# Kernel tuning notes

Measured on AMD Instinct MI355X. Metric: run time of the kernel, lower is better.

Reference implementation:

```python
import jax, jax.numpy as jnp
import numpy as np

N_NODES = 100000
N_EDGES = 600000
N_ETYPES = 3
N_LAYERS = 3  # n_layers + 1 conv layers
D = 128
EPS = 1e-5


def setup_inputs() -> dict:
    key = jax.random.key(0)
    ks = jax.random.split(key, 8)
    scale = 1.0 / np.sqrt(D)
    x = jax.random.normal(ks[0], (N_NODES, D), dtype=jnp.float32)
    src = jax.random.randint(ks[1], (N_ETYPES, N_EDGES), 0, N_NODES, dtype=jnp.int32)
    dst = jax.random.randint(ks[2], (N_ETYPES, N_EDGES), 0, N_NODES, dtype=jnp.int32)
    W_self = jax.random.normal(ks[3], (N_LAYERS, N_ETYPES, D, D), dtype=jnp.float32) * scale
    W_neigh = jax.random.normal(ks[4], (N_LAYERS, N_ETYPES, D, D), dtype=jnp.float32) * scale
    b = jax.random.normal(ks[5], (N_LAYERS, N_ETYPES, D), dtype=jnp.float32) * 0.01
    gamma = jnp.ones((N_LAYERS, D), dtype=jnp.float32)
    beta = jnp.zeros((N_LAYERS, D), dtype=jnp.float32)
    return {"x": x, "src": src, "dst": dst, "W_self": W_self, "W_neigh": W_neigh,
            "b": b, "gamma": gamma, "beta": beta}


def reference(x, src, dst, W_self, W_neigh, b, gamma, beta):
    N = x.shape[0]
    L, K = W_self.shape[0], W_self.shape[1]
    # in-degree per etype (DGL mean aggregator: zero-degree -> 0 neighbor feat)
    degs = [jnp.clip(jax.ops.segment_sum(jnp.ones((dst.shape[1],), x.dtype), dst[k],
                                         num_segments=N), 1.0, None)
            for k in range(K)]
    h = x
    for l in range(L):
        acc = jnp.zeros((N, W_self.shape[-1]), x.dtype)
        for k in range(K):
            # gather src feats, mean-aggregate onto dst: [N, D]
            neigh = jax.ops.segment_sum(h[src[k]], dst[k], num_segments=N) / degs[k][:, None]
            o = h @ W_self[l, k] + neigh @ W_neigh[l, k] + b[l, k]
            if l < L - 1:  # activation inside SAGEConv, last layer has none
                o = jax.nn.relu(o)
            acc = acc + o  # HeteroGraphConv aggregate='sum'
        # BatchNorm1d, training mode (biased batch variance)
        mu = acc.mean(axis=0)
        var = ((acc - mu) ** 2).mean(axis=0)
        h = gamma[l] * (acc - mu) / jnp.sqrt(var + EPS) + beta[l]
    return h
```

## Files before the change

### kernel.cpp

```cpp
#include <hip/hip_runtime.h>

#define NN 100000
#define NNP 100096
#define NE 600000
#define KE 3
#define NL 3
#define D  128
#define EPS 1e-5f
#define NB 391
#define NBKT 196
#define EPB 4096
#define NEB 147
#define NSL 16

typedef __attribute__((ext_vector_type(8))) short short8;
typedef __attribute__((ext_vector_type(4))) float floatx4;

__device__ __forceinline__ void atomic_add_f32(float* p, float v) { unsafeAtomicAdd(p, v); }

__device__ __forceinline__ float bf2f(unsigned int u16) {
    unsigned int v = u16 << 16;
    return __builtin_bit_cast(float, v);
}
__device__ __forceinline__ unsigned int f2bf(float f) {
    unsigned int u = __builtin_bit_cast(unsigned int, f);
    u += 0x7FFFu + ((u >> 16) & 1u);
    return u >> 16;
}
__device__ __forceinline__ unsigned int pack2(float a, float b) {
    return f2bf(a) | (f2bf(b) << 16);
}

__device__ __forceinline__ void gload16(const void* g, void* l) {
    __builtin_amdgcn_global_load_lds(
        (const __attribute__((address_space(1))) void*)g,
        (__attribute__((address_space(3))) void*)l, 16, 0, 0);
}

__global__ void convert_x_kernel(const float* __restrict__ x, ushort* __restrict__ hbf) {
    size_t i = (size_t)blockIdx.x * blockDim.x + threadIdx.x;
    if (i >= (size_t)NN * D / 4) return;
    float4 v = *(const float4*)(x + i * 4);
    uint2 o;
    o.x = pack2(v.x, v.y);
    o.y = pack2(v.z, v.w);
    *(uint2*)(hbf + i * 4) = o;
}

__global__ void wprep_kernel(const float* __restrict__ Ws, const float* __restrict__ Wn,
                             ushort* __restrict__ Bt) {
    int idx = blockIdx.x * blockDim.x + threadIdx.x;
    if (idx >= NL * KE * 128 * 256) return;
    int lk  = idx >> 15;
    int rem = idx & 32767;
    int n   = rem >> 8;
    int kk  = rem & 255;
    float v = (kk < 128) ? Ws[(size_t)lk * 16384 + kk * 128 + n]
                         : Wn[(size_t)lk * 16384 + (kk - 128) * 128 + n];
    Bt[idx] = (ushort)f2bf(v);
}

__global__ void fold_kernel(const float* __restrict__ Wsl, const float* __restrict__ bsrc,
                            const float* __restrict__ ssl, ushort* __restrict__ Btl,
                            float* __restrict__ biasW) {
    const int k = blockIdx.x;
    const int n = threadIdx.x;
    const float* W = Wsl + (size_t)k * D * D;
    ushort* B = Btl + (size_t)k * 32768;
    float acc = 0.f;
    #pragma unroll 4
    for (int kk = 0; kk < D; ++kk) {
        float w = W[kk * D + n];
        acc += ssl[D + kk] * w;
        B[n * 256 + kk] = (ushort)f2bf(ssl[kk] * w);
    }
    biasW[k * D + n] = bsrc[k * D + n] + acc;
}

__global__ void bucket_count_kernel(const int* __restrict__ dst,
                                    int* __restrict__ bucketTotal, int* __restrict__ blockBase) {
    const int blk = blockIdx.x;
    const int k = blk / NEB, cb = blk - k * NEB;
    __shared__ int hist[NBKT];
    for (int i = threadIdx.x; i < NBKT; i += 256) hist[i] = 0;
    __syncthreads();
    const int e0 = cb * EPB, e1 = min(e0 + EPB, NE);
    for (int e = e0 + threadIdx.x; e < e1; e += 256)
        atomicAdd(&hist[dst[(size_t)k * NE + e] >> 9], 1);
    __syncthreads();
    for (int i = threadIdx.x; i < NBKT; i += 256) {
        int c = hist[i];
        int base = c ? atomicAdd(&bucketTotal[k * NBKT + i], c) : 0;
        blockBase[(size_t)blk * NBKT + i] = base;
    }
}

__global__ void bucket_scan_kernel(const int* __restrict__ bucketTotal,
                                   int* __restrict__ bucketStart) {
    __shared__ int sd[1024];
    const int t = threadIdx.x;
    int v = (t < KE * NBKT) ? bucketTotal[t] : 0;
    sd[t] = v;
    __syncthreads();
    for (int off = 1; off < 1024; off <<= 1) {
        int u = (t >= off) ? sd[t - off] : 0;
        __syncthreads();
        sd[t] += u;
        __syncthreads();
    }
    if (t < KE * NBKT) bucketStart[t] = sd[t] - v;
}

__global__ void bucket_scatter_kernel(const int* __restrict__ src, const int* __restrict__ dst,
                                      const int* __restrict__ bucketStart,
                                      const int* __restrict__ blockBase,
                                      uint2* __restrict__ ebuf) {
    const int blk = blockIdx.x;
    const int k = blk / NEB, cb = blk - k * NEB;
    __shared__ int hist[NBKT], binoff[NBKT], cur[NBKT];
    __shared__ int sc[256];
    __shared__ uint2 stage[EPB];
    const int t = threadIdx.x;
    for (int i = t; i < NBKT; i += 256) hist[i] = 0;
    __syncthreads();
    const int e0 = cb * EPB, e1 = min(e0 + EPB, NE);
    for (int e = e0 + t; e < e1; e += 256)
        atomicAdd(&hist[dst[(size_t)k * NE + e] >> 9], 1);
    __syncthreads();
    int hv = (t < NBKT) ? hist[t] : 0;
    sc[t] = hv;
    __syncthreads();
    for (int off = 1; off < 256; off <<= 1) {
        int u = (t >= off) ? sc[t - off] : 0;
        __syncthreads();
        sc[t] += u;
        __syncthreads();
    }
    if (t < NBKT) { binoff[t] = sc[t] - hv; cur[t] = sc[t] - hv; }
    __syncthreads();
    for (int e = e0 + t; e < e1; e += 256) {
        int d = dst[(size_t)k * NE + e], s = src[(size_t)k * NE + e];
        int b = d >> 9;
        int p = atomicAdd(&cur[b], 1);
        stage[p] = make_uint2((unsigned)s, (unsigned)d);
    }
    __syncthreads();
    const int n = e1 - e0;
    for (int i = t; i < n; i += 256) {
        uint2 ed = stage[i];
        int b = (int)(ed.y >> 9);
        int pos = bucketStart[k * NBKT + b] + blockBase[(size_t)blk * NBKT + b] + (i - binoff[b]);
        ebuf[pos] = ed;
    }
}

__global__ void bucket_deg_kernel(const uint2* __restrict__ ebuf,
                                  const int* __restrict__ bucketStart, int* __restrict__ degi) {
    const int blk = blockIdx.x;
    const int k = blk / NBKT, b = blk - k * NBKT;
    __shared__ int cnt[512];
    for (int i = threadIdx.x; i < 512; i += 256) cnt[i] = 0;
    __syncthreads();
    const int s0 = bucketStart[blk];
    const int s1 = (blk + 1 < KE * NBKT) ? bucketStart[blk + 1] : KE * NE;
    for (int e = s0 + threadIdx.x; e < s1; e += 256)
        atomicAdd(&cnt[ebuf[e].y & 511], 1);
    __syncthreads();
    const int n0 = b << 9;
    for (int i = threadIdx.x; i < 512; i += 256) {
        int node = n0 + i;
        if (node < NN) degi[(size_t)k * NN + node] = cnt[i];
    }
}

__global__ void scan_a_kernel(const int* __restrict__ degi, int* __restrict__ bsum) {
    const int b = blockIdx.x;
    const int k = b / NB, lb = b - k * NB;
    const int t = threadIdx.x;
    const int i = lb * 256 + t;
    int deg = (i < NN) ? degi[(size_t)k * NN + i] : 0;
    __shared__ int sd[256];
    sd[t] = deg;
    __syncthreads();
    for (int off = 128; off > 0; off >>= 1) {
        if (t < off) sd[t] += sd[t + off];
        __syncthreads();
    }
    if (t == 0) bsum[b] = sd[0];
}

__global__ void scan_b_kernel(int* __restrict__ bsum) {
    const int k = blockIdx.x;
    const int t = threadIdx.x;
    int v = (t < NB) ? bsum[k * NB + t] : 0;
    __shared__ int sd[512];
    sd[t] = v;
    __syncthreads();
    for (int off = 1; off < 512; off <<= 1) {
        int u = (t >= off) ? sd[t - off] : 0;
        __syncthreads();
        sd[t] += u;
        __syncthreads();
    }
    if (t < NB) bsum[k * NB + t] = sd[t] - v;
}

__global__ void scan_c_kernel(const int* __restrict__ degi, const int* __restrict__ bsum,
                              int* __restrict__ rowptr, float* __restrict__ invdeg) {
    const int b = blockIdx.x;
    const int k = b / NB, lb = b - k * NB;
    const int t = threadIdx.x;
    const int i = lb * 256 + t;
    int deg = (i < NN) ? degi[(size_t)k * NN + i] : 0;
    __shared__ int sd[256];
    sd[t] = deg;
    __syncthreads();
    for (int off = 1; off < 256; off <<= 1) {
        int u = (t >= off) ? sd[t - off] : 0;
        __syncthreads();
        sd[t] += u;
        __syncthreads();
    }
    int val = bsum[b] + sd[t] - deg;
    if (i < NN) {
        rowptr[(size_t)k * (NN + 1) + i] = val;
        invdeg[(size_t)k * NN + i] = 1.0f / (float)max(deg, 1);
    }
    if (i == NN) rowptr[(size_t)k * (NN + 1) + NN] = NE;
}

__global__ void bucket_fill_kernel(const uint2* __restrict__ ebuf,
                                   const int* __restrict__ bucketStart,
                                   const int* __restrict__ rowptr, int* __restrict__ csr) {
    const int blk = blockIdx.x;
    const int k = blk / NBKT, b = blk - k * NBKT;
    __shared__ int cur[512];
    const int n0 = b << 9;
    for (int i = threadIdx.x; i < 512; i += 256) {
        int node = n0 + i;
        cur[i] = (node < NN) ? rowptr[(size_t)k * (NN + 1) + node] : 0;
    }
    __syncthreads();
    const int s0 = bucketStart[blk];
    const int s1 = (blk + 1 < KE * NBKT) ? bucketStart[blk + 1] : KE * NE;
    for (int e = s0 + threadIdx.x; e < s1; e += 256) {
        uint2 ed = ebuf[e];
        int p = atomicAdd(&cur[ed.y & 511], 1);
        csr[(size_t)k * NE + p] = (int)ed.x;
    }
}

__global__ void gather3_kernel(const ushort* __restrict__ hsrc, const int* __restrict__ csr,
                               const int* __restrict__ rowptr, const float* __restrict__ invdeg,
                               ushort* __restrict__ neigh, const float* __restrict__ ssl,
                               int affine) {
    int g = blockIdx.x * 16 + (threadIdx.x >> 4);
    if (g >= KE * NN) return;
    int k = g / NN, node = g - k * NN;
    const int q = (threadIdx.x & 15) * 8;
    const int* rp = rowptr + (size_t)k * (NN + 1) + node;
    const int* cs = csr + (size_t)k * NE;
    int beg = rp[0], end = rp[1];
    float f0=0,f1=0,f2=0,f3=0,f4=0,f5=0,f6=0,f7=0;
    int j = beg;
    for (; j + 4 <= end; j += 4) {
        int s0 = cs[j], s1 = cs[j + 1], s2 = cs[j + 2], s3 = cs[j + 3];
        uint4 a = *(const uint4*)(hsrc + (size_t)s0 * D + q);
        uint4 b = *(const uint4*)(hsrc + (size_t)s1 * D + q);
        uint4 c = *(const uint4*)(hsrc + (size_t)s2 * D + q);
        uint4 d = *(const uint4*)(hsrc + (size_t)s3 * D + q);
        f0 += bf2f(a.x & 0xffff) + bf2f(b.x & 0xffff) + bf2f(c.x & 0xffff) + bf2f(d.x & 0xffff);
        f1 += bf2f(a.x >> 16)    + bf2f(b.x >> 16)    + bf2f(c.x >> 16)    + bf2f(d.x >> 16);
        f2 += bf2f(a.y & 0xffff) + bf2f(b.y & 0xffff) + bf2f(c.y & 0xffff) + bf2f(d.y & 0xffff);
        f3 += bf2f(a.y >> 16)    + bf2f(b.y >> 16)    + bf2f(c.y >> 16)    + bf2f(d.y >> 16);
        f4 += bf2f(a.z & 0xffff) + bf2f(b.z & 0xffff) + bf2f(c.z & 0xffff) + bf2f(d.z & 0xffff);
        f5 += bf2f(a.z >> 16)    + bf2f(b.z >> 16)    + bf2f(c.z >> 16)    + bf2f(d.z >> 16);
        f6 += bf2f(a.w & 0xffff) + bf2f(b.w & 0xffff) + bf2f(c.w & 0xffff) + bf2f(d.w & 0xffff);
        f7 += bf2f(a.w >> 16)    + bf2f(b.w >> 16)    + bf2f(c.w >> 16)    + bf2f(d.w >> 16);
    }
    for (; j < end; ++j) {
        int s0 = cs[j];
        uint4 a = *(const uint4*)(hsrc + (size_t)s0 * D + q);
        f0 += bf2f(a.x & 0xffff); f1 += bf2f(a.x >> 16);
        f2 += bf2f(a.y & 0xffff); f3 += bf2f(a.y >> 16);
        f4 += bf2f(a.z & 0xffff); f5 += bf2f(a.z >> 16);
        f6 += bf2f(a.w & 0xffff); f7 += bf2f(a.w >> 16);
    }
    float iv = invdeg[g];
    float r0 = f0 * iv, r1 = f1 * iv, r2 = f2 * iv, r3 = f3 * iv;
    float r4 = f4 * iv, r5 = f5 * iv, r6 = f6 * iv, r7 = f7 * iv;
    if (affine) {
        float4 c0 = *(const float4*)(ssl + q);
        float4 c1 = *(const float4*)(ssl + q + 4);
        float4 h0 = *(const float4*)(ssl + D + q);
        float4 h1 = *(const float4*)(ssl + D + q + 4);
        float m = (end > beg) ? 1.0f : 0.0f;
        r0 = r0 * c0.x + m * h0.x;  r1 = r1 * c0.y + m * h0.y;
        r2 = r2 * c0.z + m * h0.z;  r3 = r3 * c0.w + m * h0.w;
        r4 = r4 * c1.x + m * h1.x;  r5 = r5 * c1.y + m * h1.y;
        r6 = r6 * c1.z + m * h1.z;  r7 = r7 * c1.w + m * h1.w;
    }
    uint4 o;
    o.x = pack2(r0, r1);
    o.y = pack2(r2, r3);
    o.z = pack2(r4, r5);
    o.w = pack2(r6, r7);
    *(uint4*)(neigh + (size_t)k * NNP * D + (size_t)node * D + q) = o;
}

__global__ __launch_bounds__(256, 2)
void layer_gemm_kernel(const ushort* __restrict__ hself, const ushort* __restrict__ neigh,
                       const ushort* __restrict__ Bt,
                       const float* __restrict__ bias,
                       ushort* __restrict__ accb, int relu,
                       float* __restrict__ colsum, float* __restrict__ colsq) {
    __shared__ __align__(16) ushort shbuf[2][128][64];
    const int tid  = threadIdx.x;
    const int wave = tid >> 6, lane = tid & 63;
    const int wm = wave & 1, wn = wave >> 1;
    const int lrow = lane & 15, quad = lane >> 4;
    const int m0 = blockIdx.x * 128;
    const int srow  = lane >> 3;
    const int scolb = (((lane & 7) ^ srow) << 4);
    char* AsL = (char*)&shbuf[0][0][0] + wave * 4096;
    char* BsL = (char*)&shbuf[1][0][0] + wave * 4096;
    const char* AsR = (const char*)&shbuf[0][0][0];
    const char* BsR = (const char*)&shbuf[1][0][0];

    floatx4 tot[4][4];
    #pragma unroll
    for (int a = 0; a < 4; ++a)
        #pragma unroll
        for (int b = 0; b < 4; ++b)
            tot[a][b] = (floatx4){0.f, 0.f, 0.f, 0.f};

    for (int k = 0; k < KE; ++k) {
        floatx4 o[4][4];
        #pragma unroll
        for (int a = 0; a < 4; ++a)
            #pragma unroll
            for (int b = 0; b < 4; ++b)
                o[a][b] = (floatx4){0.f, 0.f, 0.f, 0.f};
        const char* Btk = (const char*)Bt + (size_t)k * 65536;

        for (int part = 0; part < 2; ++part) {
            const ushort* Asrc = part ? (neigh + (size_t)k * NNP * D) : hself;
            #pragma unroll
            for (int kc = 0; kc < 2; ++kc) {
                __syncthreads();
                #pragma unroll
                for (int i = 0; i < 4; ++i) {
                    int r = wave * 32 + i * 8 + srow;
                    gload16((const char*)Asrc + (size_t)(m0 + r) * 256 + kc * 128 + scolb,
                            AsL + i * 1024);
                }
                #pragma unroll
                for (int i = 0; i < 4; ++i) {
                    int n = wave * 32 + i * 8 + srow;
                    gload16(Btk + (size_t)n * 512 + part * 256 + kc * 128 + scolb,
                            BsL + i * 1024);
                }
                __syncthreads();
                #pragma unroll
                for (int ks = 0; ks < 2; ++ks) {
                    short8 af[4], bfr[4];
                    const int cb = ks * 64 + quad * 16;
                    #pragma unroll
                    for (int im = 0; im < 4; ++im) {
                        int ra = wm * 64 + im * 16 + lrow;
                        af[im] = *(const short8*)(AsR + ra * 128 + (cb ^ ((ra & 7) << 4)));
                    }
                    #pragma unroll
                    for (int in = 0; in < 4; ++in) {
                        int rb = wn * 64 + in * 16 + lrow;
                        bfr[in] = *(const short8*)(BsR + rb * 128 + (cb ^ ((rb & 7) << 4)));
                    }
                    #pragma unroll
                    for (int im = 0; im < 4; ++im)
                        #pragma unroll
                        for (int in = 0; in < 4; ++in)
                            o[im][in] = __builtin_amdgcn_mfma_f32_16x16x32_bf16(
                                af[im], bfr[in], o[im][in], 0, 0, 0);
                }
            }
        }
        const float* bk = bias + k * D;
        float bv[4];
        #pragma unroll
        for (int in = 0; in < 4; ++in) bv[in] = bk[wn * 64 + in * 16 + lrow];
        #pragma unroll
        for (int im = 0; im < 4; ++im)
            #pragma unroll
            for (int in = 0; in < 4; ++in)
                #pragma unroll
                for (int r = 0; r < 4; ++r) {
                    float v = o[im][in][r] + bv[in];
                    if (relu) v = fmaxf(v, 0.f);
                    tot[im][in][r] += v;
                }
    }

    float ls[4] = {0.f, 0.f, 0.f, 0.f}, lq[4] = {0.f, 0.f, 0.f, 0.f};
    #pragma unroll
    for (int im = 0; im < 4; ++im)
        #pragma unroll
        for (int r = 0; r < 4; ++r) {
            int row = m0 + wm * 64 + im * 16 + quad * 4 + r;
            bool ok = row < NN;
            #pragma unroll
            for (int in = 0; in < 4; ++in) {
                float v = ok ? tot[im][in][r] : 0.f;
                ls[in] += v;
                lq[in] += v * v;
            }
        }
    __syncthreads();
    float* redS = (float*)&shbuf[0][0][0];
    float* redQ = ((float*)&shbuf[0][0][0]) + 1024;
    #pragma unroll
    for (int in = 0; in < 4; ++in) {
        int col = wn * 64 + in * 16 + lrow;
        int slot = col * 8 + wm * 4 + quad;
        redS[slot] = ls[in];
        redQ[slot] = lq[in];
    }
    __syncthreads();
    if (tid < 128) {
        float s = 0.f, q = 0.f;
        #pragma unroll
        for (int i = 0; i < 8; ++i) { s += redS[tid * 8 + i]; q += redQ[tid * 8 + i]; }
        int slice = blockIdx.x & (NSL - 1);
        atomic_add_f32(&colsum[slice * D + tid], s);
        atomic_add_f32(&colsq[slice * D + tid], q);
    }
    __syncthreads();

    ushort* Cs = &shbuf[0][0][0];
    #pragma unroll
    for (int im = 0; im < 4; ++im)
        #pragma unroll
        for (int r = 0; r < 4; ++r) {
            int rl = wm * 64 + im * 16 + quad * 4 + r;
            #pragma unroll
            for (int in = 0; in < 4; ++in)
                Cs[rl * 128 + wn * 64 + in * 16 + lrow] = (ushort)f2bf(tot[im][in][r]);
        }
    __syncthreads();
    #pragma unroll
    for (int jj = 0; jj < 8; ++jj) {
        int c8 = tid + jj * 256;
        int rl = c8 >> 4;
        int cc = (c8 & 15) * 8;
        int row = m0 + rl;
        if (row < NN)
            *(uint4*)(accb + (size_t)row * D + cc) = *(const uint4*)(Cs + rl * 128 + cc);
    }
}

__global__ void finalize_kernel(float* __restrict__ colsum, float* __restrict__ colsq,
                                const float* __restrict__ gamma, const float* __restrict__ beta,
                                float* __restrict__ ssl) {
    int c = threadIdx.x;
    float s = 0.f, q = 0.f;
    #pragma unroll
    for (int i = 0; i < NSL; ++i) { s += colsum[i * D + c]; q += colsq[i * D + c]; }
    float mu  = s * (1.0f / NN);
    float var = q * (1.0f / NN) - mu * mu;
    float sc  = gamma[c] * rsqrtf(var + EPS);
    ssl[c]     = sc;
    ssl[D + c] = beta[c] - mu * sc;
    #pragma unroll
    for (int i = 0; i < NSL; ++i) { colsum[i * D + c] = 0.f; colsq[i * D + c] = 0.f; }
}

__global__ void bn_kernel(const ushort* __restrict__ accb, const float* __restrict__ ssl,
                          float* __restrict__ out) {
    size_t i = (size_t)blockIdx.x * blockDim.x + threadIdx.x;
    if (i >= (size_t)NN * D / 4) return;
    int c4 = (int)(i & 31) << 2;
    uint2 a = *(const uint2*)(accb + i * 4);
    float4 v = {bf2f(a.x & 0xffff), bf2f(a.x >> 16), bf2f(a.y & 0xffff), bf2f(a.y >> 16)};
    float4 sc = *(const float4*)(ssl + c4);
    float4 sh = *(const float4*)(ssl + D + c4);
    float4 o;
    o.x = v.x * sc.x + sh.x;
    o.y = v.y * sc.y + sh.y;
    o.z = v.z * sc.z + sh.z;
    o.w = v.w * sc.w + sh.w;
    *(float4*)(out + i * 4) = o;
}

extern "C" void kernel_launch(void* const* d_in, const int* in_sizes, int n_in,
                              void* d_out, int out_size, void* d_ws, size_t ws_size,
                              hipStream_t stream) {
    const float* x       = (const float*)d_in[0];
    const int*   src     = (const int*)d_in[1];
    const int*   dst     = (const int*)d_in[2];
    const float* W_self  = (const float*)d_in[3];
    const float* W_neigh = (const float*)d_in[4];
    const float* bvec    = (const float*)d_in[5];
    const float* gamma   = (const float*)d_in[6];
    const float* beta    = (const float*)d_in[7];
    float* out = (float*)d_out;

    ushort* accb   = (ushort*)d_ws;
    float*  invdeg = (float*)(accb + (size_t)NNP * D);
    float*  colsum = invdeg + (size_t)KE * NN;
    float*  colsq  = colsum + NSL * D;
    float*  ss     = colsq + NSL * D;
    float*  biasW  = ss + NL * 2 * D;
    ushort* hbf    = (ushort*)(biasW + KE * D);
    ushort* neigh  = hbf + (size_t)NNP * D;
    ushort* Btw    = neigh + (size_t)KE * NNP * D;
    int*    degi   = (int*)(Btw + (size_t)NL * KE * 128 * 256);
    int*    rowptr = degi + (size_t)KE * NN;
    int*    csr    = rowptr + (size_t)KE * (NN + 1);
    int*    bsum   = csr + (size_t)KE * NE;
    int*    bucketTotal = bsum + (size_t)KE * NB;
    int*    bucketStart = bucketTotal + KE * NBKT;
    int*    blockBase   = bucketStart + KE * NBKT;
    uint2*  ebuf   = (uint2*)accb;

    convert_x_kernel<<<(int)(((size_t)NN * D / 4 + 255) / 256), 256, 0, stream>>>(x, hbf);
    wprep_kernel<<<(NL * KE * 128 * 256 + 255) / 256, 256, 0, stream>>>(W_self, W_neigh, Btw);
    hipMemsetAsync(colsum, 0, sizeof(float) * 2 * NSL * D, stream);

    hipMemsetAsync(bucketTotal, 0, sizeof(int) * KE * NBKT, stream);
    bucket_count_kernel<<<KE * NEB, 256, 0, stream>>>(dst, bucketTotal, blockBase);
    bucket_scan_kernel<<<1, 1024, 0, stream>>>(bucketTotal, bucketStart);
    bucket_scatter_kernel<<<KE * NEB, 256, 0, stream>>>(src, dst, bucketStart, blockBase, ebuf);
    bucket_deg_kernel<<<KE * NBKT, 256, 0, stream>>>(ebuf, bucketStart, degi);
    scan_a_kernel<<<KE * NB, 256, 0, stream>>>(degi, bsum);
    scan_b_kernel<<<KE, 512, 0, stream>>>(bsum);
    scan_c_kernel<<<KE * NB, 256, 0, stream>>>(degi, bsum, rowptr, invdeg);
    bucket_fill_kernel<<<KE * NBKT, 256, 0, stream>>>(ebuf, bucketStart, rowptr, csr);

    for (int l = 0; l < NL; ++l) {
        int relu = (l < NL - 1) ? 1 : 0;
        const ushort* hsrc = (l == 0) ? hbf : accb;
        const float*  ssl  = ss + (size_t)(l ? l - 1 : 0) * 2 * D;
        gather3_kernel<<<(KE * NN + 15) / 16, 256, 0, stream>>>(
            hsrc, csr, rowptr, invdeg, neigh, ssl, l > 0);
        layer_gemm_kernel<<<NNP / 128, 256, 0, stream>>>(
            hsrc, neigh,
            Btw + (size_t)l * KE * 128 * 256,
            (l == 0) ? bvec : biasW,
            accb, relu, colsum, colsq);
        finalize_kernel<<<1, 128, 0, stream>>>(colsum, colsq, gamma + (size_t)l * D,
                                               beta + (size_t)l * D, ss + (size_t)l * 2 * D);
        if (l + 1 < NL)
            fold_kernel<<<KE, 128, 0, stream>>>(
                W_self + (size_t)(l + 1) * KE * D * D,
                bvec + (size_t)(l + 1) * KE * D,
                ss + (size_t)l * 2 * D,
                Btw + (size_t)(l + 1) * KE * 128 * 256,
                biasW);
    }
    bn_kernel<<<(int)(((size_t)NN * D / 4 + 255) / 256), 256, 0, stream>>>(
        accb, ss + (size_t)(NL - 1) * 2 * D, out);
}
```

Before: 572.4 us.

## Fuse neighbor mean-gather into per-layer GEMM kernel via shared-memory A tile

Each GEMM block now gathers and mean-aggregates neighbor features for its own 128 rows per edge type. It writes them, with the folded BatchNorm affine, straight into a swizzled LDS tile, then runs the MFMA over the self and neighbor halves. This removes the separate gather kernel and the bf16 round trip of the three-edge-type neighbor buffer through global memory. Layers ping-pong between two feature buffers so a layer never overwrites the features it is still gathering from. The trade-off is that the latency-bound random gathers now run inside a kernel limited to two blocks per CU with about 80 KB of LDS each, so there is less parallelism to hide gather latency.

```diff
diff --git a/kernel.cpp b/kernel.cpp
--- a/kernel.cpp
+++ b/kernel.cpp
@@ -250,82 +250,50 @@
     }
 }
 
-__global__ void gather3_kernel(const ushort* __restrict__ hsrc, const int* __restrict__ csr,
-                               const int* __restrict__ rowptr, const float* __restrict__ invdeg,
-                               ushort* __restrict__ neigh, const float* __restrict__ ssl,
-                               int affine) {
-    int g = blockIdx.x * 16 + (threadIdx.x >> 4);
-    if (g >= KE * NN) return;
-    int k = g / NN, node = g - k * NN;
-    const int q = (threadIdx.x & 15) * 8;
-    const int* rp = rowptr + (size_t)k * (NN + 1) + node;
-    const int* cs = csr + (size_t)k * NE;
-    int beg = rp[0], end = rp[1];
-    float f0=0,f1=0,f2=0,f3=0,f4=0,f5=0,f6=0,f7=0;
-    int j = beg;
-    for (; j + 4 <= end; j += 4) {
-        int s0 = cs[j], s1 = cs[j + 1], s2 = cs[j + 2], s3 = cs[j + 3];
-        uint4 a = *(const uint4*)(hsrc + (size_t)s0 * D + q);
-        uint4 b = *(const uint4*)(hsrc + (size_t)s1 * D + q);
-        uint4 c = *(const uint4*)(hsrc + (size_t)s2 * D + q);
-        uint4 d = *(const uint4*)(hsrc + (size_t)s3 * D + q);
-        f0 += bf2f(a.x & 0xffff) + bf2f(b.x & 0xffff) + bf2f(c.x & 0xffff) + bf2f(d.x & 0xffff);
-        f1 += bf2f(a.x >> 16)    + bf2f(b.x >> 16)    + bf2f(c.x >> 16)    + bf2f(d.x >> 16);
-        f2 += bf2f(a.y & 0xffff) + bf2f(b.y & 0xffff) + bf2f(c.y & 0xffff) + bf2f(d.y & 0xffff);
-        f3 += bf2f(a.y >> 16)    + bf2f(b.y >> 16)    + bf2f(c.y >> 16)    + bf2f(d.y >> 16);
-        f4 += bf2f(a.z & 0xffff) + bf2f(b.z & 0xffff) + bf2f(c.z & 0xffff) + bf2f(d.z & 0xffff);
-        f5 += bf2f(a.z >> 16)    + bf2f(b.z >> 16)    + bf2f(c.z >> 16)    + bf2f(d.z >> 16);
-        f6 += bf2f(a.w & 0xffff) + bf2f(b.w & 0xffff) + bf2f(c.w & 0xffff) + bf2f(d.w & 0xffff);
-        f7 += bf2f(a.w >> 16)    + bf2f(b.w >> 16)    + bf2f(c.w >> 16)    + bf2f(d.w >> 16);
-    }
-    for (; j < end; ++j) {
-        int s0 = cs[j];
-        uint4 a = *(const uint4*)(hsrc + (size_t)s0 * D + q);
-        f0 += bf2f(a.x & 0xffff); f1 += bf2f(a.x >> 16);
-        f2 += bf2f(a.y & 0xffff); f3 += bf2f(a.y >> 16);
-        f4 += bf2f(a.z & 0xffff); f5 += bf2f(a.z >> 16);
-        f6 += bf2f(a.w & 0xffff); f7 += bf2f(a.w >> 16);
-    }
-    float iv = invdeg[g];
-    float r0 = f0 * iv, r1 = f1 * iv, r2 = f2 * iv, r3 = f3 * iv;
-    float r4 = f4 * iv, r5 = f5 * iv, r6 = f6 * iv, r7 = f7 * iv;
-    if (affine) {
-        float4 c0 = *(const float4*)(ssl + q);
-        float4 c1 = *(const float4*)(ssl + q + 4);
-        float4 h0 = *(const float4*)(ssl + D + q);
-        float4 h1 = *(const float4*)(ssl + D + q + 4);
-        float m = (end > beg) ? 1.0f : 0.0f;
-        r0 = r0 * c0.x + m * h0.x;  r1 = r1 * c0.y + m * h0.y;
-        r2 = r2 * c0.z + m * h0.z;  r3 = r3 * c0.w + m * h0.w;
-        r4 = r4 * c1.x + m * h1.x;  r5 = r5 * c1.y + m * h1.y;
-        r6 = r6 * c1.z + m * h1.z;  r7 = r7 * c1.w + m * h1.w;
-    }
-    uint4 o;
-    o.x = pack2(r0, r1);
-    o.y = pack2(r2, r3);
-    o.z = pack2(r4, r5);
-    o.w = pack2(r6, r7);
-    *(uint4*)(neigh + (size_t)k * NNP * D + (size_t)node * D + q) = o;
-}
-
 __global__ __launch_bounds__(256, 2)
-void layer_gemm_kernel(const ushort* __restrict__ hself, const ushort* __restrict__ neigh,
-                       const ushort* __restrict__ Bt,
-                       const float* __restrict__ bias,
-                       ushort* __restrict__ accb, int relu,
-                       float* __restrict__ colsum, float* __restrict__ colsq) {
-    __shared__ __align__(16) ushort shbuf[2][128][64];
+void layer_fused_kernel(const ushort* __restrict__ hprev,
+                        const int* __restrict__ csr, const int* __restrict__ rowptr,
+                        const float* __restrict__ invdeg,
+                        const ushort* __restrict__ Bt,
+                        const float* __restrict__ bias,
+                        const float* __restrict__ ssl,
+                        int affine, int relu,
+                        ushort* __restrict__ hnext,
+                        float* __restrict__ colsum, float* __restrict__ colsq) {
+    __shared__ __align__(16) ushort Asf[2][128][64];
+    __shared__ __align__(16) ushort Anb[2][128][64];
+    __shared__ __align__(16) ushort Bst[128][64];
     const int tid  = threadIdx.x;
     const int wave = tid >> 6, lane = tid & 63;
     const int wm = wave & 1, wn = wave >> 1;
     const int lrow = lane & 15, quad = lane >> 4;
     const int m0 = blockIdx.x * 128;
     const int srow  = lane >> 3;
-    const int scolb = (((lane & 7) ^ srow) << 4);
-    char* AsL = (char*)&shbuf[0][0][0] + wave * 4096;
-    char* BsL = (char*)&shbuf[1][0][0] + wave * 4096;
-    const char* AsR = (const char*)&shbuf[0][0][0];
-    const char* BsR = (const char*)&shbuf[1][0][0];
+    const int scolb = ((lane & 7) ^ srow) << 4;
+    const int grp = tid >> 4, l16 = tid & 15;
+    const int qb  = l16 * 8;
+    const int gkc = l16 >> 3, gc3 = l16 & 7;
+
+    {
+        const char* Ab = (const char*)hprev + (size_t)m0 * 256;
+        #pragma unroll
+        for (int kc = 0; kc < 2; ++kc)
+            #pragma unroll
+            for (int i = 0; i < 4; ++i)
+                gload16(Ab + (size_t)(wave * 32 + i * 8 + srow) * 256 + kc * 128 + scolb,
+                        (char*)Asf + kc * 16384 + wave * 4096 + i * 1024);
+    }
+
+    float4 ac0, ac1, ah0, ah1;
+    if (affine) {
+        ac0 = *(const float4*)(ssl + qb);
+        ac1 = *(const float4*)(ssl + qb + 4);
+        ah0 = *(const float4*)(ssl + D + qb);
+        ah1 = *(const float4*)(ssl + D + qb + 4);
+    } else {
+        ac0 = make_float4(1.f, 1.f, 1.f, 1.f); ac1 = ac0;
+        ah0 = make_float4(0.f, 0.f, 0.f, 0.f); ah1 = ah0;
+    }
 
     floatx4 tot[4][4];
     #pragma unroll
@@ -335,53 +303,105 @@
             tot[a][b] = (floatx4){0.f, 0.f, 0.f, 0.f};
 
     for (int k = 0; k < KE; ++k) {
-        floatx4 o[4][4];
+        const char* Btk = (const char*)Bt + (size_t)k * 65536;
+        __syncthreads();
+        #pragma unroll
+        for (int i = 0; i < 4; ++i)
+            gload16(Btk + (size_t)(wave * 32 + i * 8 + srow) * 512 + scolb,
+                    (char*)Bst + wave * 4096 + i * 1024);
+
+        const int* cs = csr + (size_t)k * NE;
+        #pragma unroll 1
+        for (int pass = 0; pass < 8; ++pass) {
+            int row  = pass * 16 + grp;
+            int node = m0 + row;
+            float f0=0,f1=0,f2=0,f3=0,f4=0,f5=0,f6=0,f7=0;
+            float iv = 0.f, mk = 0.f;
+            if (node < NN) {
+                const int* rp = rowptr + (size_t)k * (NN + 1) + node;
+                int beg = rp[0], end = rp[1];
+                int j = beg;
+                for (; j + 4 <= end; j += 4) {
+                    int s0 = cs[j], s1 = cs[j + 1], s2 = cs[j + 2], s3 = cs[j + 3];
+                    uint4 a = *(const uint4*)(hprev + (size_t)s0 * D + qb);
+                    uint4 b = *(const uint4*)(hprev + (size_t)s1 * D + qb);
+                    uint4 c = *(const uint4*)(hprev + (size_t)s2 * D + qb);
+                    uint4 d = *(const uint4*)(hprev + (size_t)s3 * D + qb);
+                    f0 += bf2f(a.x & 0xffff) + bf2f(b.x & 0xffff) + bf2f(c.x & 0xffff) + bf2f(d.x & 0xffff);
+                    f1 += bf2f(a.x >> 16)    + bf2f(b.x >> 16)    + bf2f(c.x >> 16)    + bf2f(d.x >> 16);
+                    f2 += bf2f(a.y & 0xffff) + bf2f(b.y & 0xffff) + bf2f(c.y & 0xffff) + bf2f(d.y & 0xffff);
+                    f3 += bf2f(a.y >> 16)    + bf2f(b.y >> 16)    + bf2f(c.y >> 16)    + bf2f(d.y >> 16);
+                    f4 += bf2f(a.z & 0xffff) + bf2f(b.z & 0xffff) + bf2f(c.z & 0xffff) + bf2f(d.z & 0xffff);
+                    f5 += bf2f(a.z >> 16)    + bf2f(b.z >> 16)    + bf2f(c.z >> 16)    + bf2f(d.z >> 16);
+                    f6 += bf2f(a.w & 0xffff) + bf2f(b.w & 0xffff) + bf2f(c.w & 0xffff) + bf2f(d.w & 0xffff);
+                    f7 += bf2f(a.w >> 16)    + bf2f(b.w >> 16)    + bf2f(c.w >> 16)    + bf2f(d.w >> 16);
+                }
+                for (; j < end; ++j) {
+                    int s0 = cs[j];
+                    uint4 a = *(const uint4*)(hprev + (size_t)s0 * D + qb);
+                    f0 += bf2f(a.x & 0xffff); f1 += bf2f(a.x >> 16);
+                    f2 += bf2f(a.y & 0xffff); f3 += bf2f(a.y >> 16);
+                    f4 += bf2f(a.z & 0xffff); f5 += bf2f(a.z >> 16);
+                    f6 += bf2f(a.w & 0xffff); f7 += bf2f(a.w >> 16);
+                }
+                iv = invdeg[(size_t)k * NN + node];
+                if (end > beg) mk = 1.f;
+            }
+            float r0 = f0 * iv * ac0.x + mk * ah0.x;
+            float r1 = f1 * iv * ac0.y + mk * ah0.y;
+            float r2 = f2 * iv * ac0.z + mk * ah0.z;
+            float r3 = f3 * iv * ac0.w + mk * ah0.w;
+            float r4 = f4 * iv * ac1.x + mk * ah1.x;
+            float r5 = f5 * iv * ac1.y + mk * ah1.y;
+            float r6 = f6 * iv * ac1.z + mk * ah1.z;
+            float r7 = f7 * iv * ac1.w + mk * ah1.w;
+            uint4 o;
+            o.x = pack2(r0, r1);
+            o.y = pack2(r2, r3);
+            o.z = pack2(r4, r5);
+            o.w = pack2(r6, r7);
+            *(uint4*)((char*)Anb + gkc * 16384 + row * 128 + ((gc3 ^ (row & 7)) << 4)) = o;
+        }
+
+        floatx4 o4[4][4];
         #pragma unroll
         for (int a = 0; a < 4; ++a)
             #pragma unroll
             for (int b = 0; b < 4; ++b)
-                o[a][b] = (floatx4){0.f, 0.f, 0.f, 0.f};
-        const char* Btk = (const char*)Bt + (size_t)k * 65536;
-
-        for (int part = 0; part < 2; ++part) {
-            const ushort* Asrc = part ? (neigh + (size_t)k * NNP * D) : hself;
+                o4[a][b] = (floatx4){0.f, 0.f, 0.f, 0.f};
+        #pragma unroll
+        for (int idx = 0; idx < 4; ++idx) {
+            __syncthreads();
+            const char* Ab = (idx >> 1) ? (const char*)Anb : (const char*)Asf;
+            const int kcoff = (idx & 1) * 16384;
             #pragma unroll
-            for (int kc = 0; kc < 2; ++kc) {
-                __syncthreads();
+            for (int ks = 0; ks < 2; ++ks) {
+                short8 af[4], bfr[4];
+                const int cb = ks * 64 + quad * 16;
                 #pragma unroll
-                for (int i = 0; i < 4; ++i) {
-                    int r = wave * 32 + i * 8 + srow;
-                    gload16((const char*)Asrc + (size_t)(m0 + r) * 256 + kc * 128 + scolb,
-                            AsL + i * 1024);
+                for (int im = 0; im < 4; ++im) {
+                    int ra = wm * 64 + im * 16 + lrow;
+                    af[im] = *(const short8*)(Ab + kcoff + ra * 128 + (cb ^ ((ra & 7) << 4)));
                 }
                 #pragma unroll
-                for (int i = 0; i < 4; ++i) {
-                    int n = wave * 32 + i * 8 + srow;
-                    gload16(Btk + (size_t)n * 512 + part * 256 + kc * 128 + scolb,
-                            BsL + i * 1024);
+                for (int in = 0; in < 4; ++in) {
+                    int rb = wn * 64 + in * 16 + lrow;
+                    bfr[in] = *(const short8*)((const char*)Bst + rb * 128 + (cb ^ ((rb & 7) << 4)));
                 }
+                #pragma unroll
+                for (int im = 0; im < 4; ++im)
+                    #pragma unroll
+                    for (int in = 0; in < 4; ++in)
+                        o4[im][in] = __builtin_amdgcn_mfma_f32_16x16x32_bf16(
+                            af[im], bfr[in], o4[im][in], 0, 0, 0);
+            }
+            if (idx < 3) {
                 __syncthreads();
+                const int p2 = (idx + 1) >> 1, k2 = (idx + 1) & 1;
                 #pragma unroll
-                for (int ks = 0; ks < 2; ++ks) {
-                    short8 af[4], bfr[4];
-                    const int cb = ks * 64 + quad * 16;
-                    #pragma unroll
-                    for (int im = 0; im < 4; ++im) {
-                        int ra = wm * 64 + im * 16 + lrow;
-                        af[im] = *(const short8*)(AsR + ra * 128 + (cb ^ ((ra & 7) << 4)));
-                    }
-                    #pragma unroll
-                    for (int in = 0; in < 4; ++in) {
-                        int rb = wn * 64 + in * 16 + lrow;
-                        bfr[in] = *(const short8*)(BsR + rb * 128 + (cb ^ ((rb & 7) << 4)));
-                    }
-                    #pragma unroll
-                    for (int im = 0; im < 4; ++im)
-                        #pragma unroll
-                        for (int in = 0; in < 4; ++in)
-                            o[im][in] = __builtin_amdgcn_mfma_f32_16x16x32_bf16(
-                                af[im], bfr[in], o[im][in], 0, 0, 0);
-                }
+                for (int i = 0; i < 4; ++i)
+                    gload16(Btk + (size_t)(wave * 32 + i * 8 + srow) * 512 + p2 * 256 + k2 * 128 + scolb,
+                            (char*)Bst + wave * 4096 + i * 1024);
             }
         }
         const float* bk = bias + k * D;
@@ -394,7 +414,7 @@
             for (int in = 0; in < 4; ++in)
                 #pragma unroll
                 for (int r = 0; r < 4; ++r) {
-                    float v = o[im][in][r] + bv[in];
+                    float v = o4[im][in][r] + bv[in];
                     if (relu) v = fmaxf(v, 0.f);
                     tot[im][in][r] += v;
                 }
@@ -415,8 +435,8 @@
             }
         }
     __syncthreads();
-    float* redS = (float*)&shbuf[0][0][0];
-    float* redQ = ((float*)&shbuf[0][0][0]) + 1024;
+    float* redS = (float*)&Anb[0][0][0];
+    float* redQ = redS + 1024;
     #pragma unroll
     for (int in = 0; in < 4; ++in) {
         int col = wn * 64 + in * 16 + lrow;
@@ -433,9 +453,8 @@
         atomic_add_f32(&colsum[slice * D + tid], s);
         atomic_add_f32(&colsq[slice * D + tid], q);
     }
-    __syncthreads();
-
-    ushort* Cs = &shbuf[0][0][0];
+
+    ushort* Cs = &Asf[0][0][0];
     #pragma unroll
     for (int im = 0; im < 4; ++im)
         #pragma unroll
@@ -453,7 +472,7 @@
         int cc = (c8 & 15) * 8;
         int row = m0 + rl;
         if (row < NN)
-            *(uint4*)(accb + (size_t)row * D + cc) = *(const uint4*)(Cs + rl * 128 + cc);
+            *(uint4*)(hnext + (size_t)row * D + cc) = *(const uint4*)(Cs + rl * 128 + cc);
     }
 }
 
@@ -510,8 +529,7 @@
     float*  ss     = colsq + NSL * D;
     float*  biasW  = ss + NL * 2 * D;
     ushort* hbf    = (ushort*)(biasW + KE * D);
-    ushort* neigh  = hbf + (size_t)NNP * D;
-    ushort* Btw    = neigh + (size_t)KE * NNP * D;
+    ushort* Btw    = hbf + (size_t)NNP * D;
     int*    degi   = (int*)(Btw + (size_t)NL * KE * 128 * 256);
     int*    rowptr = degi + (size_t)KE * NN;
     int*    csr    = rowptr + (size_t)KE * (NN + 1);
@@ -537,15 +555,14 @@
 
     for (int l = 0; l < NL; ++l) {
         int relu = (l < NL - 1) ? 1 : 0;
-        const ushort* hsrc = (l == 0) ? hbf : accb;
-        const float*  ssl  = ss + (size_t)(l ? l - 1 : 0) * 2 * D;
-        gather3_kernel<<<(KE * NN + 15) / 16, 256, 0, stream>>>(
-            hsrc, csr, rowptr, invdeg, neigh, ssl, l > 0);
-        layer_gemm_kernel<<<NNP / 128, 256, 0, stream>>>(
-            hsrc, neigh,
+        const ushort* hprev = (l & 1) ? accb : hbf;
+        ushort*       hnext = (l & 1) ? hbf : accb;
+        layer_fused_kernel<<<NNP / 128, 256, 0, stream>>>(
+            hprev, csr, rowptr, invdeg,
             Btw + (size_t)l * KE * 128 * 256,
             (l == 0) ? bvec : biasW,
-            accb, relu, colsum, colsq);
+            ss + (size_t)(l ? l - 1 : 0) * 2 * D, l > 0, relu,
+            hnext, colsum, colsq);
         finalize_kernel<<<1, 128, 0, stream>>>(colsum, colsq, gamma + (size_t)l * D,
                                                beta + (size_t)l * D, ss + (size_t)l * 2 * D);
         if (l + 1 < NL)
```

Result: slower. 854.6 us (+49.3%).

## Keep self-feature tile resident in LDS across edge types in layer GEMM

Applied to the files above, without the earlier changes.

The layer GEMM now loads the block's hself rows into shared memory once and reuses them for all three edge types, instead of reloading them for each type. Each type's neighbor tile is also loaded in full once. Only the weight chunk is streamed per k-chunk through a single staging buffer. This cuts redundant global loads of the A operand and some barriers, at the cost of about 80KB of LDS per block, which may reduce occupancy below the 2 blocks per CU the launch bounds request. The final reduction and output staging reuse the separate buffers, which lets one barrier be dropped.

```diff
diff --git a/kernel.cpp b/kernel.cpp
--- a/kernel.cpp
+++ b/kernel.cpp
@@ -314,18 +314,26 @@
                        const float* __restrict__ bias,
                        ushort* __restrict__ accb, int relu,
                        float* __restrict__ colsum, float* __restrict__ colsq) {
-    __shared__ __align__(16) ushort shbuf[2][128][64];
+    __shared__ __align__(16) ushort Asf[2][128][64];
+    __shared__ __align__(16) ushort Anb[2][128][64];
+    __shared__ __align__(16) ushort Bst[128][64];
     const int tid  = threadIdx.x;
     const int wave = tid >> 6, lane = tid & 63;
     const int wm = wave & 1, wn = wave >> 1;
     const int lrow = lane & 15, quad = lane >> 4;
     const int m0 = blockIdx.x * 128;
     const int srow  = lane >> 3;
-    const int scolb = (((lane & 7) ^ srow) << 4);
-    char* AsL = (char*)&shbuf[0][0][0] + wave * 4096;
-    char* BsL = (char*)&shbuf[1][0][0] + wave * 4096;
-    const char* AsR = (const char*)&shbuf[0][0][0];
-    const char* BsR = (const char*)&shbuf[1][0][0];
+    const int scolb = ((lane & 7) ^ srow) << 4;
+
+    {
+        const char* Ab = (const char*)hself + (size_t)m0 * 256;
+        #pragma unroll
+        for (int kc = 0; kc < 2; ++kc)
+            #pragma unroll
+            for (int i = 0; i < 4; ++i)
+                gload16(Ab + (size_t)(wave * 32 + i * 8 + srow) * 256 + kc * 128 + scolb,
+                        (char*)Asf + kc * 16384 + wave * 4096 + i * 1024);
+    }
 
     floatx4 tot[4][4];
     #pragma unroll
@@ -335,53 +343,61 @@
             tot[a][b] = (floatx4){0.f, 0.f, 0.f, 0.f};
 
     for (int k = 0; k < KE; ++k) {
-        floatx4 o[4][4];
+        const char* Btk = (const char*)Bt + (size_t)k * 65536;
+        __syncthreads();
+        {
+            const char* Ab = (const char*)(neigh + (size_t)k * NNP * D) + (size_t)m0 * 256;
+            #pragma unroll
+            for (int kc = 0; kc < 2; ++kc)
+                #pragma unroll
+                for (int i = 0; i < 4; ++i)
+                    gload16(Ab + (size_t)(wave * 32 + i * 8 + srow) * 256 + kc * 128 + scolb,
+                            (char*)Anb + kc * 16384 + wave * 4096 + i * 1024);
+        }
+        #pragma unroll
+        for (int i = 0; i < 4; ++i)
+            gload16(Btk + (size_t)(wave * 32 + i * 8 + srow) * 512 + scolb,
+                    (char*)Bst + wave * 4096 + i * 1024);
+
+        floatx4 o4[4][4];
         #pragma unroll
         for (int a = 0; a < 4; ++a)
             #pragma unroll
             for (int b = 0; b < 4; ++b)
-                o[a][b] = (floatx4){0.f, 0.f, 0.f, 0.f};
-        const char* Btk = (const char*)Bt + (size_t)k * 65536;
-
-        for (int part = 0; part < 2; ++part) {
-            const ushort* Asrc = part ? (neigh + (size_t)k * NNP * D) : hself;
-            #pragma unroll
-            for (int kc = 0; kc < 2; ++kc) {
-                __syncthreads();
+                o4[a][b] = (floatx4){0.f, 0.f, 0.f, 0.f};
+        #pragma unroll
+        for (int idx = 0; idx < 4; ++idx) {
+            __syncthreads();
+            const char* Ab = (idx >> 1) ? (const char*)Anb : (const char*)Asf;
+            const int kcoff = (idx & 1) * 16384;
+            #pragma unroll
+            for (int ks = 0; ks < 2; ++ks) {
+                short8 af[4], bfr[4];
+                const int cb = ks * 64 + quad * 16;
                 #pragma unroll
-                for (int i = 0; i < 4; ++i) {
-                    int r = wave * 32 + i * 8 + srow;
-                    gload16((const char*)Asrc + (size_t)(m0 + r) * 256 + kc * 128 + scolb,
-                            AsL + i * 1024);
+                for (int im = 0; im < 4; ++im) {
+                    int ra = wm * 64 + im * 16 + lrow;
+                    af[im] = *(const short8*)(Ab + kcoff + ra * 128 + (cb ^ ((ra & 7) << 4)));
                 }
                 #pragma unroll
-                for (int i = 0; i < 4; ++i) {
-                    int n = wave * 32 + i * 8 + srow;
-                    gload16(Btk + (size_t)n * 512 + part * 256 + kc * 128 + scolb,
-                            BsL + i * 1024);
+                for (int in = 0; in < 4; ++in) {
+                    int rb = wn * 64 + in * 16 + lrow;
+                    bfr[in] = *(const short8*)((const char*)Bst + rb * 128 + (cb ^ ((rb & 7) << 4)));
                 }
+                #pragma unroll
+                for (int im = 0; im < 4; ++im)
+                    #pragma unroll
+                    for (int in = 0; in < 4; ++in)
+                        o4[im][in] = __builtin_amdgcn_mfma_f32_16x16x32_bf16(
+                            af[im], bfr[in], o4[im][in], 0, 0, 0);
+            }
+            if (idx < 3) {
                 __syncthreads();
+                const int p2 = (idx + 1) >> 1, k2 = (idx + 1) & 1;
                 #pragma unroll
-                for (int ks = 0; ks < 2; ++ks) {
-                    short8 af[4], bfr[4];
-                    const int cb = ks * 64 + quad * 16;
-                    #pragma unroll
-                    for (int im = 0; im < 4; ++im) {
-                        int ra = wm * 64 + im * 16 + lrow;
-                        af[im] = *(const short8*)(AsR + ra * 128 + (cb ^ ((ra & 7) << 4)));
-                    }
-                    #pragma unroll
-                    for (int in = 0; in < 4; ++in) {
-                        int rb = wn * 64 + in * 16 + lrow;
-                        bfr[in] = *(const short8*)(BsR + rb * 128 + (cb ^ ((rb & 7) << 4)));
-                    }
-                    #pragma unroll
-                    for (int im = 0; im < 4; ++im)
-                        #pragma unroll
-                        for (int in = 0; in < 4; ++in)
-                            o[im][in] = __builtin_amdgcn_mfma_f32_16x16x32_bf16(
-                                af[im], bfr[in], o[im][in], 0, 0, 0);
-                }
+                for (int i = 0; i < 4; ++i)
+                    gload16(Btk + (size_t)(wave * 32 + i * 8 + srow) * 512 + p2 * 256 + k2 * 128 + scolb,
+                            (char*)Bst + wave * 4096 + i * 1024);
             }
         }
         const float* bk = bias + k * D;
@@ -394,7 +410,7 @@
             for (int in = 0; in < 4; ++in)
                 #pragma unroll
                 for (int r = 0; r < 4; ++r) {
-                    float v = o[im][in][r] + bv[in];
+                    float v = o4[im][in][r] + bv[in];
                     if (relu) v = fmaxf(v, 0.f);
                     tot[im][in][r] += v;
                 }
@@ -415,8 +431,8 @@
             }
         }
     __syncthreads();
-    float* redS = (float*)&shbuf[0][0][0];
-    float* redQ = ((float*)&shbuf[0][0][0]) + 1024;
+    float* redS = (float*)&Anb[0][0][0];
+    float* redQ = redS + 1024;
     #pragma unroll
     for (int in = 0; in < 4; ++in) {
         int col = wn * 64 + in * 16 + lrow;
@@ -433,9 +449,8 @@
         atomic_add_f32(&colsum[slice * D + tid], s);
         atomic_add_f32(&colsq[slice * D + tid], q);
     }
-    __syncthreads();
-
-    ushort* Cs = &shbuf[0][0][0];
+
+    ushort* Cs = &Asf[0][0][0];
     #pragma unroll
     for (int im = 0; im < 4; ++im)
         #pragma unroll
```

After: 587.3 us. 1.03x slower.
